# Kernel optimization log

Hardware: AMD Instinct MI355X
Metric: run time of the kernel (lower is better)

The kernel has to match this reference:

```python
import jax, jax.numpy as jnp
import numpy as np


def setup_inputs() -> dict:
    key = jax.random.key(0)
    k1, k2 = jax.random.split(key)
    N, T, C, HW, G = 8, 16, 256, 3136, 8
    x = jax.random.normal(k1, (N, T, C, HW), dtype=jnp.float32)
    # signed temporal shifts in [-4, 3]
    shift = jax.random.randint(k2, (N, G), 0, 8, dtype=jnp.int32) - 4
    return {"x": x, "shift": shift}


def reference(x, shift):
    """Temporal Interlace Shift.

    x:     [N, T, C, HW] feature map
    shift: [N, G] integer temporal shifts, one per channel group (G divides C)
    out[n, t, c, hw] = x[n, t + shift[n, c // (C//G)], c, hw] if the source
    frame index is in [0, T), else 0 (matches the CUDA kernel which writes
    into a zero-initialized output and skips out-of-range source frames).
    """
    N, T, C, HW = x.shape
    G = shift.shape[1]
    gc = C // G  # channels per shift group
    ch_shift = jnp.repeat(shift, gc, axis=1)  # [N, C]
    t_src = jnp.arange(T, dtype=jnp.int32)[None, :, None] + ch_shift[:, None, :]  # [N, T, C]
    valid = (t_src >= 0) & (t_src < T)  # [N, T, C]
    idx = jnp.clip(t_src, 0, T - 1)[..., None]  # [N, T, C, 1], broadcasts over HW
    out = jnp.take_along_axis(x, idx, axis=1)  # [N, T, C, HW]
    return jnp.where(valid[..., None], out, jnp.zeros((), x.dtype))
```

## Files before the change

kernel.cpp:

```cpp
#include <hip/hip_runtime.h>


#define TIN_N  8
#define TIN_T  16
#define TIN_C  256
#define TIN_HW 3136
#define TIN_G  8
#define TIN_GC (TIN_C / TIN_G)
#define TIN_HW4 (TIN_HW / 4)

__global__ __launch_bounds__(256) void tin_shift_kernel(
    const float* __restrict__ x,
    const int*   __restrict__ shift,
    float*       __restrict__ out)
{
    const int row = blockIdx.x;
    const int c   = row & (TIN_C - 1);
    const int t   = (row >> 8) & (TIN_T - 1);
    const int n   = row >> 12;

    const int g  = c >> 5;
    const int s  = shift[n * TIN_G + g];
    const int ts = t + s;

    float4*       dst = reinterpret_cast<float4*>(out) + (size_t)row * TIN_HW4;
    const int tid = threadIdx.x;

    if (ts >= 0 && ts < TIN_T) {
        const size_t src_row = ((size_t)n * TIN_T + ts) * TIN_C + c;
        const float4* src = reinterpret_cast<const float4*>(x) + src_row * TIN_HW4;
        #pragma unroll
        for (int i = tid; i < TIN_HW4; i += 256) {
            dst[i] = src[i];
        }
    } else {
        const float4 z = make_float4(0.f, 0.f, 0.f, 0.f);
        #pragma unroll
        for (int i = tid; i < TIN_HW4; i += 256) {
            dst[i] = z;
        }
    }
}

extern "C" void kernel_launch(void* const* d_in, const int* in_sizes, int n_in,
                              void* d_out, int out_size, void* d_ws, size_t ws_size,
                              hipStream_t stream)
{
    const float* x     = (const float*)d_in[0];
    const int*   shift = (const int*)d_in[1];
    float*       out   = (float*)d_out;

    const int rows = TIN_N * TIN_T * TIN_C;
    tin_shift_kernel<<<rows, 256, 0, stream>>>(x, shift, out);
}
```

Measured before the change: 141.4 us.

## Process all frames per (n,c) block with nontemporal vector loads and stores

Each block now handles one (n, c) pair across all T frames, flattening T×HW4 into an evenly divisible loop of 49 iterations instead of one row per block with a ragged tail. Loads and stores use nontemporal builtins to avoid cache pollution on this streaming copy, and out-of-range frames are handled by predication rather than separate branches. The aim is better bandwidth utilisation and less per-block overhead. The trade-off is far fewer blocks (2048), which could limit latency hiding.

```diff
diff --git a/kernel.cpp b/kernel.cpp
--- a/kernel.cpp
+++ b/kernel.cpp
@@ -1,44 +1,44 @@
 #include <hip/hip_runtime.h>
 
 
-#define TIN_N  8
-#define TIN_T  16
-#define TIN_C  256
-#define TIN_HW 3136
-#define TIN_G  8
-#define TIN_GC (TIN_C / TIN_G)
-#define TIN_HW4 (TIN_HW / 4)
+typedef float f32x4 __attribute__((ext_vector_type(4)));
+
+#define TIN_N   8
+#define TIN_T   16
+#define TIN_C   256
+#define TIN_G   8
+#define TIN_HW4 784
+#define T_STRIDE4 (TIN_C * TIN_HW4)
+#define BLK_ELEMS (TIN_T * TIN_HW4)
+#define BLK_ITERS (BLK_ELEMS / 256)
 
 __global__ __launch_bounds__(256) void tin_shift_kernel(
-    const float* __restrict__ x,
+    const f32x4* __restrict__ x4,
     const int*   __restrict__ shift,
-    float*       __restrict__ out)
+    f32x4*       __restrict__ out4)
 {
-    const int row = blockIdx.x;
-    const int c   = row & (TIN_C - 1);
-    const int t   = (row >> 8) & (TIN_T - 1);
-    const int n   = row >> 12;
+    const int nc = blockIdx.x;
+    const int c  = nc & (TIN_C - 1);
+    const int n  = nc >> 8;
+    const int s  = shift[n * TIN_G + (c >> 5)];
 
-    const int g  = c >> 5;
-    const int s  = shift[n * TIN_G + g];
-    const int ts = t + s;
+    const size_t base = ((size_t)n * (TIN_T * TIN_C) + c) * TIN_HW4;
+    const long   soff = (long)s * T_STRIDE4;
 
-    float4*       dst = reinterpret_cast<float4*>(out) + (size_t)row * TIN_HW4;
     const int tid = threadIdx.x;
 
-    if (ts >= 0 && ts < TIN_T) {
-        const size_t src_row = ((size_t)n * TIN_T + ts) * TIN_C + c;
-        const float4* src = reinterpret_cast<const float4*>(x) + src_row * TIN_HW4;
-        #pragma unroll
-        for (int i = tid; i < TIN_HW4; i += 256) {
-            dst[i] = src[i];
+    #pragma unroll 7
+    for (int it = 0; it < BLK_ITERS; ++it) {
+        const int f  = it * 256 + tid;
+        const int t  = f / TIN_HW4;
+        const int hw = f - t * TIN_HW4;
+        const size_t di = base + (size_t)t * T_STRIDE4 + (size_t)hw;
+
+        f32x4 v = (f32x4){0.f, 0.f, 0.f, 0.f};
+        if ((unsigned)(t + s) < TIN_T) {
+            v = __builtin_nontemporal_load(&x4[(long)di + soff]);
         }
-    } else {
-        const float4 z = make_float4(0.f, 0.f, 0.f, 0.f);
-        #pragma unroll
-        for (int i = tid; i < TIN_HW4; i += 256) {
-            dst[i] = z;
-        }
+        __builtin_nontemporal_store(v, &out4[di]);
     }
 }
 
@@ -46,10 +46,9 @@
                               void* d_out, int out_size, void* d_ws, size_t ws_size,
                               hipStream_t stream)
 {
-    const float* x     = (const float*)d_in[0];
+    const f32x4* x4    = (const f32x4*)d_in[0];
     const int*   shift = (const int*)d_in[1];
-    float*       out   = (float*)d_out;
+    f32x4*       out4  = (f32x4*)d_out;
 
-    const int rows = TIN_N * TIN_T * TIN_C;
-    tin_shift_kernel<<<rows, 256, 0, stream>>>(x, shift, out);
+    tin_shift_kernel<<<TIN_N * TIN_C, 256, 0, stream>>>(x4, shift, out4);
 }
```

After: 150.7 us. +6.6%, slower.
